# Kernel tuning notes

Measured on AMD Instinct MI355X. Metric: run time of the kernel, lower is better.

The kernel has to match this reference:

```python
import jax, jax.numpy as jnp
import numpy as np
import math

D_MODEL = 576
N_HEADS = 9
HEAD_DIM = D_MODEL // N_HEADS  # 64
KV_DIM = HEAD_DIM              # compression ratio 1
EPS = 1e-6


def setup_inputs() -> dict:
    key = jax.random.key(0)
    k1, k2, k3, k4 = jax.random.split(key, 4)
    B, S = 16, 2048
    x = jax.random.normal(k1, (B, S, D_MODEL), dtype=jnp.float32)
    scale = 0.02
    Wq = jax.random.normal(k2, (D_MODEL, D_MODEL), dtype=jnp.float32) * scale
    Wkv = jax.random.normal(k3, (N_HEADS * 2 * KV_DIM, D_MODEL), dtype=jnp.float32) * scale
    Wo = jax.random.normal(k4, (D_MODEL, D_MODEL), dtype=jnp.float32) * scale
    return {"x": x, "Wq": Wq, "Wkv": Wkv, "Wo": Wo}


def _rope(q):
    # q: [B, S, H, D]; rotate pairs with theta_i = 10000^{-2i/D}
    B, S, H, D = q.shape
    theta = 1.0 / (10000.0 ** (jnp.arange(0, D, 2, dtype=jnp.float32) / D))  # [D/2]
    freqs = jnp.arange(S, dtype=jnp.float32)[:, None] * theta[None, :]       # [S, D/2]
    cos = jnp.cos(freqs)[None, :, None, :]
    sin = jnp.sin(freqs)[None, :, None, :]
    qr = q.reshape(B, S, H, D // 2, 2)
    a, b = qr[..., 0], qr[..., 1]  # real / imag parts
    ra = a * cos - b * sin
    rb = a * sin + b * cos
    return jnp.stack([ra, rb], axis=-1).reshape(B, S, H, D)


def reference(x, Wq, Wkv, Wo):
    B, S, _ = x.shape
    identity = x
    # RMSNorm (weight is freshly-initialized ones in the source)
    norm = jnp.sqrt(jnp.mean(x * x, axis=-1, keepdims=True) + EPS)
    xn = x / norm
    q = (xn @ Wq.T).reshape(B, S, N_HEADS, HEAD_DIM)
    kv = (xn @ Wkv.T).reshape(B, S, N_HEADS, 2 * KV_DIM)
    k, v = kv[..., :KV_DIM], kv[..., KV_DIM:]
    q = _rope(q)
    # faithful to source: q is NOT moved to [B,H,S,D]; matmul contracts head_dim
    # per position -> head-vs-head scores [B, S, H, H]
    scores = jnp.einsum('bshd,bsgd->bshg', q, k) / math.sqrt(HEAD_DIM)
    w = jax.nn.softmax(scores.astype(jnp.float32), axis=-1).astype(x.dtype)
    attn = jnp.einsum('bshg,bsgd->bshd', w, v)  # [B, S, H, D]
    # source: transpose(1,2).contiguous().view(B, S, d_model)
    attn = jnp.transpose(attn, (0, 2, 1, 3)).reshape(B, S, D_MODEL)
    out = attn @ Wo.T
    return out + identity
```

## Files before the change

### kernel.cpp

```cpp
#include <hip/hip_runtime.h>

typedef __bf16 bf16;
typedef __attribute__((ext_vector_type(4))) float  f32x4;
typedef __attribute__((ext_vector_type(8))) short  s16x8;
typedef __attribute__((ext_vector_type(8))) __bf16 bf16x8;
typedef __attribute__((ext_vector_type(4))) __bf16 bf16x4;

#define KD    576
#define N1P   1792

#define BAR()    __builtin_amdgcn_s_barrier()
#define SCHED0() __builtin_amdgcn_sched_barrier(0)

__device__ __forceinline__ void gload_lds16(const void* g, void* l) {
  __builtin_amdgcn_global_load_lds((const __attribute__((address_space(1))) void*)g,
                                   (__attribute__((address_space(3))) void*)l, 16, 0, 0);
}

__global__ __launch_bounds__(256) void rmsnorm_k(const float* __restrict__ x,
                                                 bf16* __restrict__ xn) {
  const int lane = threadIdx.x & 63;
  const int row  = blockIdx.x * 4 + (threadIdx.x >> 6);
  const float4* xr = (const float4*)(x + (size_t)row * KD);
  float4 v0 = xr[lane];
  float4 v1 = xr[lane + 64];
  float4 v2 = {0.f, 0.f, 0.f, 0.f};
  if (lane < 16) v2 = xr[lane + 128];
  float ss = v0.x*v0.x + v0.y*v0.y + v0.z*v0.z + v0.w*v0.w
           + v1.x*v1.x + v1.y*v1.y + v1.z*v1.z + v1.w*v1.w
           + v2.x*v2.x + v2.y*v2.y + v2.z*v2.z + v2.w*v2.w;
#pragma unroll
  for (int off = 32; off > 0; off >>= 1) ss += __shfl_xor(ss, off, 64);
  const float inv = 1.0f / sqrtf(ss * (1.0f / 576.0f) + 1e-6f);
  bf16* orow = xn + (size_t)row * KD;
  bf16x4 o0 = {(bf16)(v0.x*inv), (bf16)(v0.y*inv), (bf16)(v0.z*inv), (bf16)(v0.w*inv)};
  *(bf16x4*)(orow + lane * 4) = o0;
  bf16x4 o1 = {(bf16)(v1.x*inv), (bf16)(v1.y*inv), (bf16)(v1.z*inv), (bf16)(v1.w*inv)};
  *(bf16x4*)(orow + (lane + 64) * 4) = o1;
  if (lane < 16) {
    bf16x4 o2 = {(bf16)(v2.x*inv), (bf16)(v2.y*inv), (bf16)(v2.z*inv), (bf16)(v2.w*inv)};
    *(bf16x4*)(orow + (lane + 128) * 4) = o2;
  }
}

__global__ void ropetab_k(float* __restrict__ ctab, float* __restrict__ stab) {
  const int s = blockIdx.x * blockDim.x + threadIdx.x;
  if (s >= 2048) return;
  const float l2r = 0.4152410118609203f;
#pragma unroll 1
  for (int i = 0; i < 32; ++i) {
    const float theta = exp2f(-(float)i * l2r);
    const float f = (float)s * theta;
    float sv, cv;
    sincosf(f, &sv, &cv);
    ctab[s * 32 + i] = cv;
    stab[s * 32 + i] = sv;
  }
}

__global__ __launch_bounds__(256) void wconv_k(const float* __restrict__ Wq,
                                               const float* __restrict__ Wkv,
                                               const float* __restrict__ Wo,
                                               bf16* __restrict__ wcat,
                                               bf16* __restrict__ wo) {
  const int idx = blockIdx.x * 256 + threadIdx.x;
  {
    const int row = idx / 576;
    float v = 0.f;
    if (row < 576)       v = Wq[idx];
    else if (row < 1728) v = Wkv[idx - 331776];
    wcat[idx] = (bf16)v;
  }
  if (idx < 640 * 576) {
    float v = (idx < 331776) ? Wo[idx] : 0.f;
    wo[idx] = (bf16)v;
  }
}

__global__ __launch_bounds__(512, 2) void gemm8p_k(const bf16* __restrict__ A,
                                                   const bf16* __restrict__ Bw,
                                                   bf16* __restrict__ C,
                                                   int ntiles) {
  extern __shared__ char smem[];
  const int tid  = threadIdx.x;
  const int lane = tid & 63;
  const int wv   = tid >> 6;
  const int nwg = gridDim.x;
  const int cpx = nwg >> 3;
  const int swz = (blockIdx.x & 7) * cpx + (blockIdx.x >> 3);
  const int mt = swz / ntiles;
  const int nt = swz - mt * ntiles;
  const int wMl = (wv >> 2) << 7;
  const int wNl = (wv & 3) << 6;

  const bf16* Ab = A  + (size_t)mt * 256 * KD;
  const bf16* Bb = Bw + (size_t)nt * 256 * KD;

  int off[4];
#pragma unroll
  for (int u = 0; u < 2; ++u)
#pragma unroll
    for (int q = 0; q < 2; ++q) {
      const int c = u * 1024 + q * 512 + tid;
      const int row = c >> 3, slot = c & 7;
      const int ks = slot ^ (row & 7);
      off[u * 2 + q] = row * KD + ks * 8;
    }

  auto stage_unit = [&](int uu, int k0n, int bb) {
    const int u = uu & 1;
#pragma unroll
    for (int q = 0; q < 2; ++q) {
      const int c = u * 1024 + q * 512 + tid;
      if (uu < 2) gload_lds16(Ab + off[u * 2 + q] + k0n, smem + bb * 65536 + c * 16);
      else        gload_lds16(Bb + off[u * 2 + q] + k0n, smem + bb * 65536 + 32768 + c * 16);
    }
  };

  f32x4 acc[8][4];
#pragma unroll
  for (int i = 0; i < 8; ++i)
#pragma unroll
    for (int j = 0; j < 4; ++j) { acc[i][j][0]=0.f; acc[i][j][1]=0.f; acc[i][j][2]=0.f; acc[i][j][3]=0.f; }

#pragma unroll
  for (int uu = 0; uu < 4; ++uu) stage_unit(uu, 0, 0);

#pragma unroll 1
  for (int t = 0; t < 9; ++t) {
    const int cur = t & 1, nxt = cur ^ 1;
    const int k0n = (t + 1) * 64;
    if (t < 8) {
      stage_unit(0, k0n, nxt);
      stage_unit(1, k0n, nxt);
      asm volatile("s_waitcnt vmcnt(4)" ::: "memory");
    } else {
      asm volatile("s_waitcnt vmcnt(0)" ::: "memory");
    }
    BAR();
    const bf16* As = (const bf16*)(smem + cur * 65536);
    const bf16* Bs = (const bf16*)(smem + cur * 65536 + 32768);
    s16x8 bfrag[4][2];
#pragma unroll
    for (int p = 0; p < 4; ++p) {
      s16x8 afrag[2][2];
#pragma unroll
      for (int i2 = 0; i2 < 2; ++i2)
#pragma unroll
        for (int kk = 0; kk < 2; ++kk) {
          const int arow = wMl + (p * 2 + i2) * 16 + (lane & 15);
          const int aps  = ((kk << 2) + (lane >> 4)) ^ (arow & 7);
          afrag[i2][kk] = *(const s16x8*)(As + arow * 64 + aps * 8);
        }
      if (p == 0) {
#pragma unroll
        for (int j = 0; j < 4; ++j)
#pragma unroll
          for (int kk = 0; kk < 2; ++kk) {
            const int brow = wNl + j * 16 + (lane & 15);
            const int bps  = ((kk << 2) + (lane >> 4)) ^ (brow & 7);
            bfrag[j][kk] = *(const s16x8*)(Bs + brow * 64 + bps * 8);
          }
      }
      if (t < 8 && p < 2) stage_unit(2 + p, k0n, nxt);
      asm volatile("s_waitcnt lgkmcnt(0)" ::: "memory");
      SCHED0();
      __builtin_amdgcn_s_setprio(1);
#pragma unroll
      for (int i2 = 0; i2 < 2; ++i2)
#pragma unroll
        for (int j = 0; j < 4; ++j)
#pragma unroll
          for (int kk = 0; kk < 2; ++kk)
            acc[p * 2 + i2][j] = __builtin_amdgcn_mfma_f32_16x16x32_bf16(
                afrag[i2][kk], bfrag[j][kk], acc[p * 2 + i2][j], 0, 0, 0);
      __builtin_amdgcn_s_setprio(0);
      SCHED0();
    }
    BAR();
  }

  bf16* ep = (bf16*)(smem + wv * 9216);
  const size_t crow0 = (size_t)(mt * 256 + wMl);
  const int    ccol0 = nt * 256 + wNl;
#pragma unroll
  for (int half = 0; half < 2; ++half) {
    asm volatile("s_waitcnt lgkmcnt(0)" ::: "memory"); SCHED0();
#pragma unroll
    for (int i = 0; i < 4; ++i)
#pragma unroll
      for (int j = 0; j < 4; ++j)
#pragma unroll
        for (int r = 0; r < 4; ++r) {
          const int row = i * 16 + ((lane >> 4) << 2) + r;
          ep[row * 72 + j * 16 + (lane & 15)] = (bf16)acc[half * 4 + i][j][r];
        }
    asm volatile("s_waitcnt lgkmcnt(0)" ::: "memory"); SCHED0();
#pragma unroll
    for (int it = 0; it < 8; ++it) {
      const int c = it * 64 + lane;
      const int row = c >> 3, c8 = c & 7;
      s16x8 v = *(const s16x8*)(ep + row * 72 + c8 * 8);
      *(s16x8*)(C + (crow0 + half * 64 + row) * (size_t)N1P + ccol0 + c8 * 8) = v;
    }
  }
}

__global__ __launch_bounds__(256) void gemm_o_k(const bf16* __restrict__ A,
                                                const bf16* __restrict__ Bw,
                                                float* __restrict__ C,
                                                const float* __restrict__ ident,
                                                int ntiles) {
  __shared__ bf16 As[128 * 64];
  __shared__ bf16 Bs[128 * 64];
  const int tid  = threadIdx.x;
  const int lane = tid & 63;
  const int nwg = gridDim.x;
  const int cpx = nwg >> 3;
  const int swz = (blockIdx.x & 7) * cpx + (blockIdx.x >> 3);
  const int mt = swz / ntiles;
  const int nt = swz - mt * ntiles;
  const int wv = tid >> 6;
  const int wr = (wv >> 1) << 6;
  const int wc = (wv & 1) << 6;

  const size_t abase = (size_t)mt * 128 * KD;
  const size_t bbase = (size_t)nt * 128 * KD;

  f32x4 zero = {0.f, 0.f, 0.f, 0.f};
  f32x4 acc[4][4];
#pragma unroll
  for (int i = 0; i < 4; ++i)
#pragma unroll
    for (int j = 0; j < 4; ++j) acc[i][j] = zero;

  for (int kt = 0; kt < 9; ++kt) {
    const int k0 = kt * 64;
    __syncthreads();
#pragma unroll
    for (int r = 0; r < 4; ++r) {
      const int c   = r * 256 + tid;
      const int row = c >> 3;
      const int ks  = (c & 7) ^ (row & 7);
      gload_lds16(A + abase + (size_t)row * KD + k0 + ks * 8, As + c * 8);
    }
#pragma unroll
    for (int r = 0; r < 4; ++r) {
      const int c   = r * 256 + tid;
      const int row = c >> 3;
      const int ks  = (c & 7) ^ (row & 7);
      gload_lds16(Bw + bbase + (size_t)row * KD + k0 + ks * 8, Bs + c * 8);
    }
    __syncthreads();
#pragma unroll
    for (int kk = 0; kk < 2; ++kk) {
      s16x8 af[4], bq[4];
#pragma unroll
      for (int i = 0; i < 4; ++i) {
        const int arow = wr + i * 16 + (lane & 15);
        const int aps  = ((kk << 2) + (lane >> 4)) ^ (arow & 7);
        af[i] = *(const s16x8*)(As + arow * 64 + aps * 8);
      }
#pragma unroll
      for (int j = 0; j < 4; ++j) {
        const int brow = wc + j * 16 + (lane & 15);
        const int bps  = ((kk << 2) + (lane >> 4)) ^ (brow & 7);
        bq[j] = *(const s16x8*)(Bs + brow * 64 + bps * 8);
      }
#pragma unroll
      for (int i = 0; i < 4; ++i)
#pragma unroll
        for (int j = 0; j < 4; ++j)
          acc[i][j] = __builtin_amdgcn_mfma_f32_16x16x32_bf16(af[i], bq[j], acc[i][j], 0, 0, 0);
    }
  }
  const int rbase = mt * 128 + wr + ((lane >> 4) << 2);
  const int cbase = nt * 128 + wc + (lane & 15);
#pragma unroll
  for (int i = 0; i < 4; ++i)
#pragma unroll
    for (int j = 0; j < 4; ++j) {
      const int col = cbase + j * 16;
      if (col < 576) {
#pragma unroll
        for (int r = 0; r < 4; ++r) {
          const size_t o = (size_t)(rbase + i * 16 + r) * 576 + col;
          C[o] = acc[i][j][r] + ident[o];
        }
      }
    }
}

__global__ __launch_bounds__(256) void attn2_k(const bf16* __restrict__ qkv,
                                               const float* __restrict__ ctab,
                                               const float* __restrict__ stab,
                                               bf16* __restrict__ attn) {
  const int tid = blockIdx.x * 256 + threadIdx.x;
  const int bs  = tid / 9;
  const int h   = tid - bs * 9;
  const int s   = bs & 2047;
  const bf16* qrow = qkv + (size_t)bs * N1P;

  float q[64];
#pragma unroll
  for (int c = 0; c < 8; ++c) {
    bf16x8 v = *(const bf16x8*)(qrow + h * 64 + c * 8);
#pragma unroll
    for (int e = 0; e < 8; ++e) q[c * 8 + e] = (float)v[e];
  }
  const float* cr = ctab + s * 32;
  const float* sr = stab + s * 32;
#pragma unroll
  for (int i = 0; i < 32; ++i) {
    const float cv = cr[i], sv = sr[i];
    const float a = q[2 * i], b = q[2 * i + 1];
    q[2 * i]     = a * cv - b * sv;
    q[2 * i + 1] = a * sv + b * cv;
  }
  const bf16* kvr = qrow + 576;
  float sc[9];
#pragma unroll
  for (int g = 0; g < 9; ++g) {
    const bf16* kg = kvr + g * 128;
    float d0 = 0.f, d1 = 0.f, d2 = 0.f, d3 = 0.f;
#pragma unroll
    for (int c = 0; c < 8; ++c) {
      bf16x8 v = *(const bf16x8*)(kg + c * 8);
      d0 += q[c*8+0] * (float)v[0];
      d1 += q[c*8+1] * (float)v[1];
      d2 += q[c*8+2] * (float)v[2];
      d3 += q[c*8+3] * (float)v[3];
      d0 += q[c*8+4] * (float)v[4];
      d1 += q[c*8+5] * (float)v[5];
      d2 += q[c*8+6] * (float)v[6];
      d3 += q[c*8+7] * (float)v[7];
    }
    sc[g] = (d0 + d1 + d2 + d3) * 0.125f;
  }
  float mx = sc[0];
#pragma unroll
  for (int g = 1; g < 9; ++g) mx = fmaxf(mx, sc[g]);
  float sum = 0.f;
#pragma unroll
  for (int g = 0; g < 9; ++g) { sc[g] = expf(sc[g] - mx); sum += sc[g]; }
  const float inv = 1.0f / sum;
#pragma unroll
  for (int g = 0; g < 9; ++g) sc[g] *= inv;

  const int b = bs >> 11;
  bf16* orow = attn + ((size_t)((b * 9 + h) * 2048 + s)) * 64;
#pragma unroll
  for (int c = 0; c < 8; ++c) {
    float o[8];
#pragma unroll
    for (int e = 0; e < 8; ++e) o[e] = 0.f;
#pragma unroll
    for (int g = 0; g < 9; ++g) {
      bf16x8 v = *(const bf16x8*)(kvr + g * 128 + 64 + c * 8);
#pragma unroll
      for (int e = 0; e < 8; ++e) o[e] += sc[g] * (float)v[e];
    }
    bf16x8 ov;
#pragma unroll
    for (int e = 0; e < 8; ++e) ov[e] = (bf16)o[e];
    *(bf16x8*)(orow + c * 8) = ov;
  }
}

extern "C" void kernel_launch(void* const* d_in, const int* in_sizes, int n_in,
                              void* d_out, int out_size, void* d_ws, size_t ws_size,
                              hipStream_t stream) {
  const float* x   = (const float*)d_in[0];
  const float* Wq  = (const float*)d_in[1];
  const float* Wkv = (const float*)d_in[2];
  const float* Wo  = (const float*)d_in[3];

  char* ws = (char*)d_ws;
  const size_t o_xn   = 0;
  const size_t o_wcat = o_xn   + 37748736;
  const size_t o_wo   = o_wcat + 2064384;
  const size_t o_ct   = o_wo   + 737280;
  const size_t o_st   = o_ct   + 262144;
  const size_t o_qkv  = o_st   + 262144;
  const size_t need   = o_qkv  + 117440512;
  if (ws_size < need) return;

  bf16*  xn   = (bf16*)(ws + o_xn);
  bf16*  attn = (bf16*)(ws + o_xn);
  bf16*  wcat = (bf16*)(ws + o_wcat);
  bf16*  wo   = (bf16*)(ws + o_wo);
  float* ctab = (float*)(ws + o_ct);
  float* stab = (float*)(ws + o_st);
  bf16*  qkv  = (bf16*)(ws + o_qkv);

  hipFuncSetAttribute((const void*)gemm8p_k,
                      hipFuncAttributeMaxDynamicSharedMemorySize, 131072);

  rmsnorm_k<<<8192, 256, 0, stream>>>(x, xn);
  ropetab_k<<<32, 64, 0, stream>>>(ctab, stab);
  wconv_k<<<4032, 256, 0, stream>>>(Wq, Wkv, Wo, wcat, wo);
  gemm8p_k<<<896, 512, 131072, stream>>>(xn, wcat, qkv, 7);
  attn2_k<<<1152, 256, 0, stream>>>(qkv, ctab, stab, attn);
  gemm_o_k<<<1280, 256, 0, stream>>>(attn, wo, (float*)d_out, x, 5);
}
```

Measured before the change: 341.5 us.

## Stage attention rows in LDS and vectorize output GEMM epilogue via shared memory

The attention kernel now loads 16 full qkv rows per block into LDS with direct global-to-LDS loads, and each position's 9 heads are served by threads reading from LDS. This replaces scattered, uncoalesced per-thread global reads. The output GEMM epilogue now stages accumulators through LDS so it can do float4-vectorized residual loads and output stores instead of scalar strided ones. The cost is that 7 of every 16 attention threads sit idle, the attention kernel needs more LDS per block, and the epilogue adds extra synchronization.

```diff
diff --git a/kernel.cpp b/kernel.cpp
--- a/kernel.cpp
+++ b/kernel.cpp
@@ -211,8 +211,9 @@
                                                 float* __restrict__ C,
                                                 const float* __restrict__ ident,
                                                 int ntiles) {
-  __shared__ bf16 As[128 * 64];
-  __shared__ bf16 Bs[128 * 64];
+  __shared__ bf16 smem2[2 * 128 * 64];
+  bf16* As = smem2;
+  bf16* Bs = smem2 + 128 * 64;
   const int tid  = threadIdx.x;
   const int lane = tid & 63;
   const int nwg = gridDim.x;
@@ -274,37 +275,62 @@
           acc[i][j] = __builtin_amdgcn_mfma_f32_16x16x32_bf16(af[i], bq[j], acc[i][j], 0, 0, 0);
     }
   }
-  const int rbase = mt * 128 + wr + ((lane >> 4) << 2);
-  const int cbase = nt * 128 + wc + (lane & 15);
-#pragma unroll
-  for (int i = 0; i < 4; ++i)
-#pragma unroll
-    for (int j = 0; j < 4; ++j) {
-      const int col = cbase + j * 16;
-      if (col < 576) {
-#pragma unroll
-        for (int r = 0; r < 4; ++r) {
-          const size_t o = (size_t)(rbase + i * 16 + r) * 576 + col;
-          C[o] = acc[i][j][r] + ident[o];
-        }
+
+  __syncthreads();
+  float* ep = (float*)smem2 + wv * (16 * 68);
+  const int rgrp = lane >> 4;
+  const int lc   = lane & 15;
+  const bool colsOK = (nt * 128 + wc) < 576;
+#pragma unroll
+  for (int i = 0; i < 4; ++i) {
+#pragma unroll
+    for (int j = 0; j < 4; ++j)
+#pragma unroll
+      for (int r = 0; r < 4; ++r)
+        ep[(rgrp * 4 + r) * 68 + j * 16 + lc] = acc[i][j][r];
+    asm volatile("s_waitcnt lgkmcnt(0)" ::: "memory"); SCHED0();
+    if (colsOK) {
+#pragma unroll
+      for (int p = 0; p < 4; ++p) {
+        const int rr  = p * 4 + rgrp;
+        const int row = mt * 128 + wr + i * 16 + rr;
+        const int col = nt * 128 + wc + lc * 4;
+        f32x4 v = *(const f32x4*)(ep + rr * 68 + lc * 4);
+        const float4 id = *(const float4*)(ident + (size_t)row * 576 + col);
+        v[0] += id.x; v[1] += id.y; v[2] += id.z; v[3] += id.w;
+        *(f32x4*)(C + (size_t)row * 576 + col) = v;
       }
     }
-}
-
-__global__ __launch_bounds__(256) void attn2_k(const bf16* __restrict__ qkv,
+    asm volatile("s_waitcnt lgkmcnt(0)" ::: "memory"); SCHED0();
+  }
+}
+
+__global__ __launch_bounds__(256) void attn3_k(const bf16* __restrict__ qkv,
                                                const float* __restrict__ ctab,
                                                const float* __restrict__ stab,
                                                bf16* __restrict__ attn) {
-  const int tid = blockIdx.x * 256 + threadIdx.x;
-  const int bs  = tid / 9;
-  const int h   = tid - bs * 9;
-  const int s   = bs & 2047;
-  const bf16* qrow = qkv + (size_t)bs * N1P;
+  __shared__ bf16 lds[16 * 1800];
+  const int tid = threadIdx.x;
+  const int bs0 = blockIdx.x << 4;
+  if (tid < 216) {
+#pragma unroll
+    for (int row = 0; row < 16; ++row)
+      gload_lds16(qkv + (size_t)(bs0 + row) * N1P + tid * 8, lds + row * 1800 + tid * 8);
+  }
+  __syncthreads();
+
+  const int pos = tid >> 4;
+  const int w   = tid & 15;
+  if (w >= 9) return;
+  const int bs = bs0 + pos;
+  const int s  = bs & 2047;
+  const int b  = bs >> 11;
+  const bf16* qrow = lds + pos * 1800;
 
   float q[64];
 #pragma unroll
   for (int c = 0; c < 8; ++c) {
-    bf16x8 v = *(const bf16x8*)(qrow + h * 64 + c * 8);
+    bf16x8 v = *(const bf16x8*)(qrow + w * 64 + c * 8);
 #pragma unroll
     for (int e = 0; e < 8; ++e) q[c * 8 + e] = (float)v[e];
   }
@@ -313,9 +339,9 @@
 #pragma unroll
   for (int i = 0; i < 32; ++i) {
     const float cv = cr[i], sv = sr[i];
-    const float a = q[2 * i], b = q[2 * i + 1];
-    q[2 * i]     = a * cv - b * sv;
-    q[2 * i + 1] = a * sv + b * cv;
+    const float a = q[2 * i], bq_ = q[2 * i + 1];
+    q[2 * i]     = a * cv - bq_ * sv;
+    q[2 * i + 1] = a * sv + bq_ * cv;
   }
   const bf16* kvr = qrow + 576;
   float sc[9];
@@ -347,8 +373,7 @@
 #pragma unroll
   for (int g = 0; g < 9; ++g) sc[g] *= inv;
 
-  const int b = bs >> 11;
-  bf16* orow = attn + ((size_t)((b * 9 + h) * 2048 + s)) * 64;
+  bf16* orow = attn + ((size_t)((b * 9 + w) * 2048 + s)) * 64;
 #pragma unroll
   for (int c = 0; c < 8; ++c) {
     float o[8];
@@ -400,6 +425,6 @@
   ropetab_k<<<32, 64, 0, stream>>>(ctab, stab);
   wconv_k<<<4032, 256, 0, stream>>>(Wq, Wkv, Wo, wcat, wo);
   gemm8p_k<<<896, 512, 131072, stream>>>(xn, wcat, qkv, 7);
-  attn2_k<<<1152, 256, 0, stream>>>(qkv, ctab, stab, attn);
+  attn3_k<<<2048, 256, 0, stream>>>(qkv, ctab, stab, attn);
   gemm_o_k<<<1280, 256, 0, stream>>>(attn, wo, (float*)d_out, x, 5);
 }
```

New measurement: 332.2 us. 2.7% less time.
